# Kernel tuning notes

Hardware: AMD Instinct MI355X
Metric: run time of the kernel (lower is better)

## Reference

```python
import jax, jax.numpy as jnp
import numpy as np

# Model hyperparameters (match init_kwargs)
J, L, A, A_PRIME = 5, 4, 4, 1
M = N = 128
C = 1
NB = 2
DELTA_J, DELTA_L = J, L
MASK_ANGLES = 4
SHIFT_R = 4  # radius (pixels) of directional correlation shifts
EPS = 1e-6


def _pair_indices():
    """Static (i1, i2) indices into the flattened [C*J*L*A] coefficient axis
    for cross-scale/angle correlation pairs: j1 <= j2 <= j1+delta_j,
    circular |l1-l2| <= delta_l, a1 in [0,A), a2 in [0,A_prime)."""
    i1, i2 = [], []
    flat = lambda c, j, l, a: ((c * J + j) * L + l) * A + a
    for c in range(C):
        for j1 in range(J):
            for j2 in range(j1, min(j1 + DELTA_J, J - 1) + 1):
                for l1 in range(L):
                    for l2 in range(L):
                        dl = min((l1 - l2) % L, (l2 - l1) % L)
                        if dl > DELTA_L:
                            continue
                        for a1 in range(A):
                            for a2 in range(A_PRIME):
                                i1.append(flat(c, j1, l1, a1))
                                i2.append(flat(c, j2, l2, a2))
    return np.asarray(i1, np.int32), np.asarray(i2, np.int32)


def _shifts():
    """Zero shift plus MASK_ANGLES directional shifts at radius SHIFT_R."""
    sh = [(0, 0)]
    for s in range(MASK_ANGLES):
        th = np.pi * s / MASK_ANGLES
        sh.append((int(round(SHIFT_R * np.cos(th))), int(round(SHIFT_R * np.sin(th)))))
    return sh


def _highpass_filters():
    """Angular-sector highpass masks in Fourier space: |k| > pi/2 split into
    MASK_ANGLES orientation sectors (angle folded to [0, pi))."""
    kx = 2 * np.pi * np.fft.fftfreq(M)[:, None]
    ky = 2 * np.pi * np.fft.fftfreq(N)[None, :]
    r = np.sqrt(kx ** 2 + ky ** 2)
    th = np.mod(np.arctan2(ky, kx), np.pi)
    h = []
    for s in range(MASK_ANGLES):
        lo, hi = np.pi * s / MASK_ANGLES, np.pi * (s + 1) / MASK_ANGLES
        h.append(((r > np.pi / 2) & (th >= lo) & (th < hi)).astype(np.float32))
    return np.stack(h)  # [MASK_ANGLES, M, N]


def setup_inputs() -> dict:
    key = jax.random.key(0)
    k = jax.random.split(key, 5)
    return {
        "x": jax.random.normal(k[0], (NB, C, M, N), jnp.float32),
        "hatpsi_re": jax.random.normal(k[1], (C, J, L, A, M, N), jnp.float32),
        "hatpsi_im": jax.random.normal(k[2], (C, J, L, A, M, N), jnp.float32),
        "hatphi_re": jax.random.normal(k[3], (M, N), jnp.float32),
        "hatphi_im": jax.random.normal(k[4], (M, N), jnp.float32),
    }


def reference(x, hatpsi_re, hatpsi_im, hatphi_re, hatphi_im):
    nb = x.shape[0]
    # --- WaveConvLayer: FFT wavelet convolution ---
    hatx = jnp.fft.fft2(x)  # [nb, C, M, N] complex
    hatpsi = hatpsi_re + 1j * hatpsi_im  # [C, J, L, A, M, N]
    xpsi = jnp.fft.ifft2(hatx[:, :, None, None, None] * hatpsi[None])  # [nb,C,J,L,A,M,N]
    # --- ReluCenterLayer: ReLU of real part, spatially centered, L2-normalized ---
    y = jax.nn.relu(xpsi.real)
    y = y - y.mean((-2, -1), keepdims=True)
    y = y / (jnp.sqrt((y * y).mean((-2, -1), keepdims=True)) + EPS)
    yf = y.reshape(nb, C * J * L * A, M, N)
    # --- CorrLayer: shifted cross-correlations over pair list ---
    i1, i2 = _pair_indices()
    a1 = yf[:, i1].reshape(nb, -1, M * N)  # [nb, P, M*N]
    a2 = yf[:, i2]                          # [nb, P, M, N]
    corrs = []
    for (dx, dy) in _shifts():  # small fixed set of shifts
        a2r = jnp.roll(a2, (dx, dy), axis=(-2, -1)).reshape(nb, -1, M * N)
        corrs.append(jnp.einsum('npx,npx->np', a1, a2r) / (M * N))
    xcorr = jnp.concatenate(corrs, axis=1)  # [nb, P * n_shifts]
    # --- LowpassLayer: phi-filtered moments (mean, mean-square) ---
    hatphi = hatphi_re + 1j * hatphi_im
    xlow_map = jnp.fft.ifft2(hatx * hatphi).real  # [nb, C, M, N]
    xlow = jnp.stack([xlow_map.mean((-2, -1)), (xlow_map ** 2).mean((-2, -1))], axis=-1)  # [nb,C,2]
    # --- HighpassLayer: per-sector highpass energy (Parseval) ---
    hhigh = jnp.asarray(_highpass_filters())  # [MASK_ANGLES, M, N]
    xhigh = (jnp.abs(hatx[:, :, None] * hhigh) ** 2).mean((-2, -1)) / (M * N)  # [nb,C,MASK_ANGLES]
    return jnp.concatenate([xcorr, xlow.reshape(nb, -1), xhigh.reshape(nb, -1)], axis=1)
```

## Files before the change

kernel.cpp:

```cpp
#include <hip/hip_runtime.h>
#include <math.h>

#define NB 2
#define NMAPS 81
#define NPSI 80
#define PIXELS 16384
#define OUT_STRIDE 4806

constexpr double PI_D = 3.14159265358979323846;

__device__ inline float2 cmulf(float2 a, float2 b) {
  return make_float2(a.x * b.x - a.y * b.y, a.x * b.y + a.y * b.x);
}

template <int CTRL>
__device__ inline float dppf(float v) {
  return __int_as_float(
      __builtin_amdgcn_update_dpp(0, __float_as_int(v), CTRL, 0xf, 0xf, true));
}

__device__ inline float shx(float v, const int mask) {
  if (mask == 1) return dppf<0xB1>(v);
  if (mask == 2) return dppf<0x4E>(v);
  if (mask == 8) return dppf<0x128>(v);
  if (mask == 32) {
    auto r = __builtin_amdgcn_permlane32_swap(__float_as_uint(v),
                                              __float_as_uint(v), false, false);
    return __uint_as_float((threadIdx.x & 32) ? r[0] : r[1]);
  }
  return __shfl_xor(v, mask);
}

__device__ inline float wred64(float v) {
  int x;
  x = __builtin_amdgcn_update_dpp(0, __float_as_int(v), 0x111, 0xf, 0xf, true); v += __int_as_float(x);
  x = __builtin_amdgcn_update_dpp(0, __float_as_int(v), 0x112, 0xf, 0xf, true); v += __int_as_float(x);
  x = __builtin_amdgcn_update_dpp(0, __float_as_int(v), 0x114, 0xf, 0xf, true); v += __int_as_float(x);
  x = __builtin_amdgcn_update_dpp(0, __float_as_int(v), 0x118, 0xf, 0xf, true); v += __int_as_float(x);
  x = __builtin_amdgcn_update_dpp(0, __float_as_int(v), 0x142, 0xa, 0xf, true); v += __int_as_float(x);
  x = __builtin_amdgcn_update_dpp(0, __float_as_int(v), 0x143, 0xc, 0xf, true); v += __int_as_float(x);
  return __int_as_float(__builtin_amdgcn_readlane(__float_as_int(v), 63));
}


__global__ __launch_bounds__(128) void k_fft_rows(const float* __restrict__ x,
                                                  float2* __restrict__ tx,
                                                  int* __restrict__ sector) {
  const int tid = threadIdx.x;
  const int blkid = blockIdx.x;
  if (blkid >= NB * 128) {
    int idx = (blkid - NB * 128) * 128 + tid;
    int i = idx >> 7, j = idx & 127;
    double fx = (double)(i < 64 ? i : i - 128) / 128.0;
    double fy = (double)(j < 64 ? j : j - 128) / 128.0;
    double kx = (2.0 * PI_D) * fx;
    double ky = (2.0 * PI_D) * fy;
    double r2 = kx * kx + ky * ky;
    const double h = PI_D / 2.0;
    int s = -1;
    if (r2 > h * h) {
      double th = atan2(ky, kx);
      th = fmod(th, PI_D);
      if (th < 0.0) th += PI_D;
      if (th < PI_D * 0.25) s = 0;
      else if (th < PI_D * 0.5) s = 1;
      else if (th < PI_D * 0.75) s = 2;
      else if (th < PI_D) s = 3;
    }
    sector[idx] = s;
    return;
  }
  __shared__ float row[128];
  __shared__ float2 wt[128];
  const int m = blkid & 127;
  const int b = blkid >> 7;
  {
    double ang = -(2.0 * PI_D / 128.0) * (double)tid;
    wt[tid] = make_float2((float)cos(ang), (float)sin(ang));
  }
  row[tid] = x[(b << 14) + (m << 7) + tid];
  __syncthreads();
  float ar = 0.f, ai = 0.f;
  int idx = 0;
  const int v = tid;
#pragma unroll 8
  for (int n = 0; n < 128; ++n) {
    float xv = row[n];
    float2 w = wt[idx];
    ar = fmaf(xv, w.x, ar);
    ai = fmaf(xv, w.y, ai);
    idx = (idx + v) & 127;
  }
  tx[(b << 14) + (m << 7) + tid] = make_float2(ar, ai);
}

__global__ __launch_bounds__(128) void k_fft_cols(const float2* __restrict__ tx,
                                                  float2* __restrict__ hatx) {
  __shared__ float2 col[128];
  __shared__ float2 wt[128];
  const int tid = threadIdx.x;
  const int v = blockIdx.x & 127;
  const int b = blockIdx.x >> 7;
  {
    double ang = -(2.0 * PI_D / 128.0) * (double)tid;
    wt[tid] = make_float2((float)cos(ang), (float)sin(ang));
  }
  col[tid] = tx[(b << 14) + (tid << 7) + v];
  __syncthreads();
  float ar = 0.f, ai = 0.f;
  int idx = 0;
  const int u = tid;
#pragma unroll 8
  for (int mm = 0; mm < 128; ++mm) {
    float2 z = col[mm];
    float2 w = wt[idx];
    ar += z.x * w.x - z.y * w.y;
    ai += z.x * w.y + z.y * w.x;
    idx = (idx + u) & 127;
  }
  hatx[(b << 14) + (tid << 7) + v] = make_float2(ar, ai);
}

#define BFLY(z)                                     \
  {                                                 \
    float tx_ = shx((z).x, mask);                   \
    float ty_ = shx((z).y, mask);                   \
    float ax_ = fmaf(s, (z).x, tx_);                \
    float ay_ = fmaf(s, (z).y, ty_);                \
    (z).x = ax_ * we.x - ay_ * we.y;                \
    (z).y = ax_ * we.y + ay_ * we.x;                \
  }

__device__ inline void fft128_inv(float2& z0, float2& z1, float2& z2, float2& z3,
                                  const float2* __restrict__ wt, int l) {
  {
    float2 w = wt[l];
    float2 a0 = make_float2(z0.x + z1.x, z0.y + z1.y);
    float2 d0 = make_float2(z0.x - z1.x, z0.y - z1.y);
    z0 = a0;
    z1 = cmulf(d0, w);
    float2 a1 = make_float2(z2.x + z3.x, z2.y + z3.y);
    float2 d1 = make_float2(z2.x - z3.x, z2.y - z3.y);
    z2 = a1;
    z3 = cmulf(d1, w);
  }
#pragma unroll
  for (int mask = 32; mask >= 1; mask >>= 1) {
    float2 w = wt[(l & (mask - 1)) * (64 / mask)];
    const bool up = (l & mask) != 0;
    const float s = up ? -1.f : 1.f;
    const float2 we = up ? w : make_float2(1.f, 0.f);
    BFLY(z0);
    BFLY(z1);
    BFLY(z2);
    BFLY(z3);
  }
}


__global__ __launch_bounds__(1024) void k_ifft2d(
    const float2* __restrict__ hatx,
    const float* __restrict__ psi_re, const float* __restrict__ psi_im,
    const float* __restrict__ phi_re, const float* __restrict__ phi_im,
    float* __restrict__ y, float2* __restrict__ meaninv,
    float* __restrict__ out) {
  __shared__ float2 Tsh[128 * 129];
  __shared__ float2 wt[64];
  __shared__ float2 red16[16];
  const int tid = threadIdx.x;
  const int l = tid & 63;
  const int w = tid >> 6;
  const int mf = blockIdx.x;
  const int b = mf / NMAPS;
  const int f = mf - b * NMAPS;
  if (tid < 64) {
    double ang = (2.0 * PI_D / 128.0) * (double)tid;
    wt[tid] = make_float2((float)cos(ang), (float)sin(ang));
  }
  __syncthreads();
  const float2* hb2 = hatx + (b << 14);
  const float* fre = (f < NPSI) ? psi_re + ((size_t)f << 14) : phi_re;
  const float* fim = (f < NPSI) ? psi_im + ((size_t)f << 14) : phi_im;
  {
    const int sl = (l >> 4) & 3;
    float2 H[4][4];
    float FR[4][4], FI[4][4];
#pragma unroll
    for (int r = 0; r < 4; ++r) {
      const int o = (r * 32 + (w << 1)) << 7;
      H[r][0] = hb2[o + l];
      H[r][1] = hb2[o + l + 64];
      H[r][2] = hb2[o + 128 + l];
      H[r][3] = hb2[o + 128 + l + 64];
    }
#pragma unroll
    for (int r = 0; r < 4; ++r) {
      const int o = (r * 32 + (w << 1)) << 7;
      FR[r][0] = fre[o + l];            FI[r][0] = fim[o + l];
      FR[r][1] = fre[o + l + 64];       FI[r][1] = fim[o + l + 64];
      FR[r][2] = fre[o + 128 + l];      FI[r][2] = fim[o + 128 + l];
      FR[r][3] = fre[o + 128 + l + 64]; FI[r][3] = fim[o + 128 + l + 64];
    }
#pragma unroll
    for (int r = 0; r < 4; ++r) {
      const int uA = r * 32 + (w << 1);
      float2 zA0 = cmulf(H[r][0], make_float2(FR[r][0], FI[r][0]));
      float2 zA1 = cmulf(H[r][1], make_float2(FR[r][1], FI[r][1]));
      float2 zB0 = cmulf(H[r][2], make_float2(FR[r][2], FI[r][2]));
      float2 zB1 = cmulf(H[r][3], make_float2(FR[r][3], FI[r][3]));
      fft128_inv(zA0, zA1, zB0, zB1, wt, l);
      Tsh[l * 129 + (uA ^ sl)] = zA0;
      Tsh[(l + 64) * 129 + (uA ^ sl)] = zA1;
      Tsh[l * 129 + ((uA + 1) ^ sl)] = zB0;
      Tsh[(l + 64) * 129 + ((uA + 1) ^ sl)] = zB1;
    }
  }
  __syncthreads();
  float s1 = 0.f, s2 = 0.f;
  float* yb = y + ((size_t)(b * NPSI + f) << 14);
  const int m2 = __brev(l) >> 26;
  const int um  = (128 - l) & 127;
  const int um2 = (64 - l) & 127;
  for (int r = 0; r < 2; ++r) {
    const int q0 = r * 64 + (w << 2);
    const int sq = (q0 >> 4) & 3;
    const int li = l ^ sq;
    const int umi = um ^ sq;
    const int um2i = um2 ^ sq;
    float2 zA0, zA1, zB0, zB1;
    {
      const float2* C0 = &Tsh[(q0    ) * 129];
      const float2* C1 = &Tsh[(q0 + 1) * 129];
      float2 a0 = C0[li], a0m = C0[umi], a1 = C0[li + 64], a1m = C0[um2i];
      float2 b0 = C1[li], b0m = C1[umi], b1 = C1[li + 64], b1m = C1[um2i];
      zA0 = make_float2(0.5f * (a0.x + a0m.x) - 0.5f * (b0.y - b0m.y),
                        0.5f * (a0.y - a0m.y) + 0.5f * (b0.x + b0m.x));
      zA1 = make_float2(0.5f * (a1.x + a1m.x) - 0.5f * (b1.y - b1m.y),
                        0.5f * (a1.y - a1m.y) + 0.5f * (b1.x + b1m.x));
      const float2* C2 = &Tsh[(q0 + 2) * 129];
      const float2* C3 = &Tsh[(q0 + 3) * 129];
      float2 c0 = C2[li], c0m = C2[umi], c1 = C2[li + 64], c1m = C2[um2i];
      float2 d0 = C3[li], d0m = C3[umi], d1 = C3[li + 64], d1m = C3[um2i];
      zB0 = make_float2(0.5f * (c0.x + c0m.x) - 0.5f * (d0.y - d0m.y),
                        0.5f * (c0.y - c0m.y) + 0.5f * (d0.x + d0m.x));
      zB1 = make_float2(0.5f * (c1.x + c1m.x) - 0.5f * (d1.y - d1m.y),
                        0.5f * (c1.y - c1m.y) + 0.5f * (d1.x + d1m.x));
    }
    fft128_inv(zA0, zA1, zB0, zB1, wt, l);
    const float sc = 1.f / 16384.f;
    const int nA0 = __brev(q0) >> 25;
    float xA00 = zA0.x * sc, xA01 = zA0.y * sc;
    float xA10 = zA1.x * sc, xA11 = zA1.y * sc;
    float xB00 = zB0.x * sc, xB01 = zB0.y * sc;
    float xB10 = zB1.x * sc, xB11 = zB1.y * sc;
    if (f < NPSI) {
      xA00 = fmaxf(xA00, 0.f); xA01 = fmaxf(xA01, 0.f);
      xA10 = fmaxf(xA10, 0.f); xA11 = fmaxf(xA11, 0.f);
      xB00 = fmaxf(xB00, 0.f); xB01 = fmaxf(xB01, 0.f);
      xB10 = fmaxf(xB10, 0.f); xB11 = fmaxf(xB11, 0.f);
      *(float2*)(yb + ((nA0     ) << 7) + (m2 << 1)) = make_float2(xA00, xA10);
      *(float2*)(yb + ((nA0 + 64) << 7) + (m2 << 1)) = make_float2(xA01, xA11);
      *(float2*)(yb + ((nA0 + 32) << 7) + (m2 << 1)) = make_float2(xB00, xB10);
      *(float2*)(yb + ((nA0 + 96) << 7) + (m2 << 1)) = make_float2(xB01, xB11);
    }
    s1 += xA00 + xA01 + xA10 + xA11 + xB00 + xB01 + xB10 + xB11;
    s2 += xA00 * xA00 + xA01 * xA01 + xA10 * xA10 + xA11 * xA11 +
          xB00 * xB00 + xB01 * xB01 + xB10 * xB10 + xB11 * xB11;
  }
  float t1 = wred64(s1), t2 = wred64(s2);
  if (l == 0) red16[w] = make_float2(t1, t2);
  __syncthreads();
  if (w == 0) {
    float2 p = (l < 16) ? red16[l] : make_float2(0.f, 0.f);
    float S1 = wred64(p.x), S2 = wred64(p.y);
    if (l == 0) {
      float mean = S1 * (1.f / 16384.f);
      float msq  = S2 * (1.f / 16384.f);
      if (f < NPSI) {
        float var = fmaxf(msq - mean * mean, 0.f);
        meaninv[b * NPSI + f] = make_float2(mean, 1.f / (sqrtf(var) + 1e-6f));
      } else {
        out[b * OUT_STRIDE + 4800] = mean;
        out[b * OUT_STRIDE + 4801] = msq;
      }
    }
  }
}

__global__ __launch_bounds__(256) void k_corrtail(
    const float* __restrict__ y, const float2* __restrict__ meaninv,
    const float2* __restrict__ hatx, const int* __restrict__ sector,
    float* __restrict__ out) {
  const int tid = threadIdx.x;
  const int l = tid & 63;
  const int w = tid >> 6;
  const int work = ((blockIdx.x & 7) * 61) + (blockIdx.x >> 3);
  if (work >= NB * 240) {
    const int b = work - NB * 240;
    if (b >= NB) return;
    __shared__ float red[4][4];
    float a0 = 0, a1 = 0, a2 = 0, a3 = 0;
    for (int k = tid; k < PIXELS; k += 256) {
      float2 hx = hatx[(b << 14) + k];
      float mag = hx.x * hx.x + hx.y * hx.y;
      int s = sector[k];
      if (s == 0) a0 += mag;
      else if (s == 1) a1 += mag;
      else if (s == 2) a2 += mag;
      else if (s == 3) a3 += mag;
    }
    a0 = wred64(a0); a1 = wred64(a1); a2 = wred64(a2); a3 = wred64(a3);
    if (l == 0) { red[w][0] = a0; red[w][1] = a1; red[w][2] = a2; red[w][3] = a3; }
    __syncthreads();
    if (tid < 4) {
      float tot = red[0][tid] + red[1][tid] + red[2][tid] + red[3][tid];
      out[b * OUT_STRIDE + 4802 + tid] = tot * (1.f / (16384.f * 16384.f));
    }
    return;
  }
  __shared__ float s2m[128 * 132];
  __shared__ float redb[4 * 20];
  __shared__ float2 mi[5];
  const int b = work / 240;
  const int r_ = work - b * 240;
  const int jj = r_ >> 4;
  const int l1 = (r_ >> 2) & 3;
  const int l2 = r_ & 3;
  int j1 = 0, rem = jj;
  while (rem >= 5 - j1) { rem -= (5 - j1); ++j1; }
  const int j2 = j1 + rem;
  const int i1b = j1 * 16 + l1 * 4;
  const int i2 = j2 * 16 + l2 * 4;
  if (tid < 4) mi[tid] = meaninv[b * NPSI + i1b + tid];
  else if (tid == 4) mi[4] = meaninv[b * NPSI + i2];
  const float* __restrict__ y1 = y + ((size_t)(b * NPSI + i1b) << 14);
  const float* __restrict__ y2 = y + ((size_t)(b * NPSI + i2) << 14);
  const int r0 = tid >> 5;
  const int c4 = (tid & 31) << 2;
#pragma unroll
  for (int k = 0; k < 16; ++k) {
    int row = k * 8 + r0;
    *(float4*)&s2m[row * 132 + c4] = *(const float4*)&y2[(row << 7) + c4];
  }
  __syncthreads();
  if (tid < 128) {
    *(float4*)&s2m[tid * 132 + 128] = *(const float4*)&s2m[tid * 132];
  }
  __syncthreads();
  const int bm4 = (c4 + 124) & 127;
  float acc[20];
#pragma unroll
  for (int o = 0; o < 20; ++o) acc[o] = 0.f;
#pragma unroll 4
  for (int k = 0; k < 16; ++k) {
    const int r = k * 8 + r0;
    const int rm0 = r * 132;
    const int rm3 = ((r + 125) & 127) * 132;
    const int rm4 = ((r + 124) & 127) * 132;
    float4 q0 = *(const float4*)&s2m[rm0 + c4];
    float4 q1 = *(const float4*)&s2m[rm0 + bm4];
    float4 q3 = *(const float4*)&s2m[rm4 + c4];
    float4 qa = *(const float4*)&s2m[rm3 + bm4];
    float4 qb = *(const float4*)&s2m[rm3 + bm4 + 4];
    float4 qd = *(const float4*)&s2m[rm3 + c4 + 4];
    const float u2x = qa.y, u2y = qa.z, u2z = qa.w, u2w = qb.x;
    const float u4x = qb.w, u4y = qd.x, u4z = qd.y, u4w = qd.z;
#pragma unroll
    for (int m = 0; m < 4; ++m) {
      float4 v = *(const float4*)&y1[(m << 14) + (r << 7) + c4];
      acc[m*5+0] = fmaf(v.w,q0.w,fmaf(v.z,q0.z,fmaf(v.y,q0.y,fmaf(v.x,q0.x,acc[m*5+0]))));
      acc[m*5+1] = fmaf(v.w,q1.w,fmaf(v.z,q1.z,fmaf(v.y,q1.y,fmaf(v.x,q1.x,acc[m*5+1]))));
      acc[m*5+2] = fmaf(v.w,u2w,fmaf(v.z,u2z,fmaf(v.y,u2y,fmaf(v.x,u2x,acc[m*5+2]))));
      acc[m*5+3] = fmaf(v.w,q3.w,fmaf(v.z,q3.z,fmaf(v.y,q3.y,fmaf(v.x,q3.x,acc[m*5+3]))));
      acc[m*5+4] = fmaf(v.w,u4w,fmaf(v.z,u4z,fmaf(v.y,u4y,fmaf(v.x,u4x,acc[m*5+4]))));
    }
  }
#pragma unroll
  for (int o = 0; o < 20; ++o) {
    float tot = wred64(acc[o]);
    if (l == 0) redb[w * 20 + o] = tot;
  }
  __syncthreads();
  if (tid < 20) {
    int m = tid / 5, s = tid - m * 5;
    float tot = redb[tid] + redb[20 + tid] + redb[40 + tid] + redb[60 + tid];
    float2 m1 = mi[m], m2 = mi[4];
    float c = m1.y * m2.y * (tot * (1.f / 16384.f) - m1.x * m2.x);
    int p = jj * 64 + l1 * 16 + l2 * 4 + m;
    out[b * OUT_STRIDE + s * 960 + p] = c;
  }
}

extern "C" void kernel_launch(void* const* d_in, const int* in_sizes, int n_in,
                              void* d_out, int out_size, void* d_ws, size_t ws_size,
                              hipStream_t stream) {
  (void)in_sizes; (void)n_in; (void)out_size; (void)ws_size;
  const float* x      = (const float*)d_in[0];
  const float* psi_re = (const float*)d_in[1];
  const float* psi_im = (const float*)d_in[2];
  const float* phi_re = (const float*)d_in[3];
  const float* phi_im = (const float*)d_in[4];
  float* out = (float*)d_out;
  char* ws = (char*)d_ws;

  constexpr size_t TX_BYTES   = (size_t)NB * PIXELS * sizeof(float2);
  constexpr size_t HATX_OFF   = TX_BYTES;
  constexpr size_t HATX_BYTES = (size_t)NB * PIXELS * sizeof(float2);
  constexpr size_t Y_OFF      = HATX_OFF + HATX_BYTES;
  constexpr size_t Y_BYTES    = (size_t)NB * NPSI * PIXELS * sizeof(float);
  constexpr size_t MI_OFF     = Y_OFF + Y_BYTES;
  constexpr size_t MI_BYTES   = (size_t)NB * NPSI * sizeof(float2);
  constexpr size_t SEC_OFF    = MI_OFF + MI_BYTES;

  float2* tx       = (float2*)(ws);
  float2* hatx     = (float2*)(ws + HATX_OFF);
  float*  y        = (float*)(ws + Y_OFF);
  float2* meaninv  = (float2*)(ws + MI_OFF);
  int*    sector   = (int*)(ws + SEC_OFF);

  k_fft_rows<<<NB * 128 + 128, 128, 0, stream>>>(x, tx, sector);
  k_fft_cols<<<NB * 128, 128, 0, stream>>>(tx, hatx);
  k_ifft2d<<<NB * NMAPS, 1024, 0, stream>>>(hatx, psi_re, psi_im, phi_re, phi_im,
                                            y, meaninv, out);
  k_corrtail<<<488, 256, 0, stream>>>(y, meaninv, hatx, sector, out);
}
```

Before: 57.60 us.

## Hermitian-symmetrize spectrum before first IFFT pass to halve row transforms

Instead of running the full 128-row inverse FFT and extracting the real part in the second pass, the kernel forms the Hermitian-symmetric part of the product spectrum up front, loading each point together with its mirror. Because that part has a real inverse transform, only 65 rows need the first pass, and shared memory shrinks from 128x129 to 65x129 entries. The column pass then rebuilds the packed pairs from a row and its mirror row. This roughly halves first-stage FFT work and LDS footprint, at the cost of twice as many global loads per point, including scattered mirror-index loads.

```diff
diff --git a/kernel.cpp b/kernel.cpp
--- a/kernel.cpp
+++ b/kernel.cpp
@@ -164,7 +164,7 @@
     const float* __restrict__ phi_re, const float* __restrict__ phi_im,
     float* __restrict__ y, float2* __restrict__ meaninv,
     float* __restrict__ out) {
-  __shared__ float2 Tsh[128 * 129];
+  __shared__ float2 Tsh[65 * 129];
   __shared__ float2 wt[64];
   __shared__ float2 red16[16];
   const int tid = threadIdx.x;
@@ -181,71 +181,61 @@
   const float2* hb2 = hatx + (b << 14);
   const float* fre = (f < NPSI) ? psi_re + ((size_t)f << 14) : phi_re;
   const float* fim = (f < NPSI) ? psi_im + ((size_t)f << 14) : phi_im;
-  {
-    const int sl = (l >> 4) & 3;
-    float2 H[4][4];
-    float FR[4][4], FI[4][4];
-#pragma unroll
-    for (int r = 0; r < 4; ++r) {
-      const int o = (r * 32 + (w << 1)) << 7;
-      H[r][0] = hb2[o + l];
-      H[r][1] = hb2[o + l + 64];
-      H[r][2] = hb2[o + 128 + l];
-      H[r][3] = hb2[o + 128 + l + 64];
-    }
-#pragma unroll
-    for (int r = 0; r < 4; ++r) {
-      const int o = (r * 32 + (w << 1)) << 7;
-      FR[r][0] = fre[o + l];            FI[r][0] = fim[o + l];
-      FR[r][1] = fre[o + l + 64];       FI[r][1] = fim[o + l + 64];
-      FR[r][2] = fre[o + 128 + l];      FI[r][2] = fim[o + 128 + l];
-      FR[r][3] = fre[o + 128 + l + 64]; FI[r][3] = fim[o + 128 + l + 64];
-    }
-#pragma unroll
-    for (int r = 0; r < 4; ++r) {
-      const int uA = r * 32 + (w << 1);
-      float2 zA0 = cmulf(H[r][0], make_float2(FR[r][0], FI[r][0]));
-      float2 zA1 = cmulf(H[r][1], make_float2(FR[r][1], FI[r][1]));
-      float2 zB0 = cmulf(H[r][2], make_float2(FR[r][2], FI[r][2]));
-      float2 zB1 = cmulf(H[r][3], make_float2(FR[r][3], FI[r][3]));
-      fft128_inv(zA0, zA1, zB0, zB1, wt, l);
-      Tsh[l * 129 + (uA ^ sl)] = zA0;
-      Tsh[(l + 64) * 129 + (uA ^ sl)] = zA1;
-      Tsh[l * 129 + ((uA + 1) ^ sl)] = zB0;
-      Tsh[(l + 64) * 129 + ((uA + 1) ^ sl)] = zB1;
-    }
-  }
+  const int vr0 = (128 - l) & 127;
+  const int vr1 = (64 - l) & 127;
+#define LOADZ(u, v) cmulf(hb2[((u) << 7) + (v)], \
+    make_float2(fre[((u) << 7) + (v)], fim[((u) << 7) + (v)]))
+  for (int r = 0; r < 2; ++r) {
+    const int uA = r * 32 + (w << 1);
+    const int uB = uA + 1;
+    const int uAr = (128 - uA) & 127;
+    const int uBr = 128 - uB;
+    float2 dA0 = LOADZ(uA, l),        dA1 = LOADZ(uA, l + 64);
+    float2 mA0 = LOADZ(uAr, vr0),     mA1 = LOADZ(uAr, vr1);
+    float2 dB0 = LOADZ(uB, l),        dB1 = LOADZ(uB, l + 64);
+    float2 mB0 = LOADZ(uBr, vr0),     mB1 = LOADZ(uBr, vr1);
+    float2 wA0 = make_float2(0.5f * (dA0.x + mA0.x), 0.5f * (dA0.y - mA0.y));
+    float2 wA1 = make_float2(0.5f * (dA1.x + mA1.x), 0.5f * (dA1.y - mA1.y));
+    float2 wB0 = make_float2(0.5f * (dB0.x + mB0.x), 0.5f * (dB0.y - mB0.y));
+    float2 wB1 = make_float2(0.5f * (dB1.x + mB1.x), 0.5f * (dB1.y - mB1.y));
+    fft128_inv(wA0, wA1, wB0, wB1, wt, l);
+    const int su = (uA >> 4) & 3;
+    Tsh[uA * 129 + (l ^ su)] = wA0;
+    Tsh[uA * 129 + ((l ^ su) + 64)] = wA1;
+    Tsh[uB * 129 + (l ^ su)] = wB0;
+    Tsh[uB * 129 + ((l ^ su) + 64)] = wB1;
+  }
+  if (w == 0) {
+    float2 d0 = LOADZ(64, l), d1 = LOADZ(64, l + 64);
+    float2 m0 = LOADZ(64, vr0), m1 = LOADZ(64, vr1);
+    float2 w0 = make_float2(0.5f * (d0.x + m0.x), 0.5f * (d0.y - m0.y));
+    float2 w1 = make_float2(0.5f * (d1.x + m1.x), 0.5f * (d1.y - m1.y));
+    float2 w2 = w0, w3 = w1;
+    fft128_inv(w0, w1, w2, w3, wt, l);
+    Tsh[64 * 129 + l] = w0;
+    Tsh[64 * 129 + l + 64] = w1;
+  }
+#undef LOADZ
   __syncthreads();
   float s1 = 0.f, s2 = 0.f;
   float* yb = y + ((size_t)(b * NPSI + f) << 14);
   const int m2 = __brev(l) >> 26;
-  const int um  = (128 - l) & 127;
-  const int um2 = (64 - l) & 127;
+  const int rm = 64 - l;
+  const int sl = (l >> 4) & 3;
+  const int sm = (rm >> 4) & 3;
+  const float sgn = (l == 0) ? 1.f : -1.f;
+  const float2* rowL = &Tsh[l * 129];
+  const float2* rowM = &Tsh[rm * 129];
   for (int r = 0; r < 2; ++r) {
     const int q0 = r * 64 + (w << 2);
-    const int sq = (q0 >> 4) & 3;
-    const int li = l ^ sq;
-    const int umi = um ^ sq;
-    const int um2i = um2 ^ sq;
-    float2 zA0, zA1, zB0, zB1;
-    {
-      const float2* C0 = &Tsh[(q0    ) * 129];
-      const float2* C1 = &Tsh[(q0 + 1) * 129];
-      float2 a0 = C0[li], a0m = C0[umi], a1 = C0[li + 64], a1m = C0[um2i];
-      float2 b0 = C1[li], b0m = C1[umi], b1 = C1[li + 64], b1m = C1[um2i];
-      zA0 = make_float2(0.5f * (a0.x + a0m.x) - 0.5f * (b0.y - b0m.y),
-                        0.5f * (a0.y - a0m.y) + 0.5f * (b0.x + b0m.x));
-      zA1 = make_float2(0.5f * (a1.x + a1m.x) - 0.5f * (b1.y - b1m.y),
-                        0.5f * (a1.y - a1m.y) + 0.5f * (b1.x + b1m.x));
-      const float2* C2 = &Tsh[(q0 + 2) * 129];
-      const float2* C3 = &Tsh[(q0 + 3) * 129];
-      float2 c0 = C2[li], c0m = C2[umi], c1 = C2[li + 64], c1m = C2[um2i];
-      float2 d0 = C3[li], d0m = C3[umi], d1 = C3[li + 64], d1m = C3[um2i];
-      zB0 = make_float2(0.5f * (c0.x + c0m.x) - 0.5f * (d0.y - d0m.y),
-                        0.5f * (c0.y - c0m.y) + 0.5f * (d0.x + d0m.x));
-      zB1 = make_float2(0.5f * (c1.x + c1m.x) - 0.5f * (d1.y - d1m.y),
-                        0.5f * (c1.y - c1m.y) + 0.5f * (d1.x + d1m.x));
-    }
+    float2 a  = rowL[(q0    ) ^ sl], bb = rowL[(q0 + 1) ^ sl];
+    float2 c  = rowL[(q0 + 2) ^ sl], d  = rowL[(q0 + 3) ^ sl];
+    float2 am = rowM[(q0    ) ^ sm], bm = rowM[(q0 + 1) ^ sm];
+    float2 cm = rowM[(q0 + 2) ^ sm], dm = rowM[(q0 + 3) ^ sm];
+    float2 zA0 = make_float2(a.x - bb.y, a.y + bb.x);
+    float2 zA1 = make_float2(fmaf(-sgn, bm.y, am.x), fmaf(sgn, am.y, bm.x));
+    float2 zB0 = make_float2(c.x - d.y, c.y + d.x);
+    float2 zB1 = make_float2(fmaf(-sgn, dm.y, cm.x), fmaf(sgn, cm.y, dm.x));
     fft128_inv(zA0, zA1, zB0, zB1, wt, l);
     const float sc = 1.f / 16384.f;
     const int nA0 = __brev(q0) >> 25;
```

Result: faster. 54.78 us (-4.9%).
